# Optimization experiments

Hardware: AMD Instinct MI355X
Metric: run time of the kernel (lower is better)

The kernel has to match this reference:

```python
import jax, jax.numpy as jnp
import numpy as np
import math

B, TQ, TK, C, H, DFF = 4, 1024, 1024, 1024, 16, 4096
DK = C // H
EPS = 1e-12


def _mha(x_q, x_kv, wq, bq, wk, bk, wv, bv, wo, bo, mask):
    Bq, Tq, Cq = x_q.shape
    Tk = x_kv.shape[1]
    q = (x_q @ wq + bq).reshape(Bq, Tq, H, DK).transpose(0, 2, 1, 3)  # [B,H,Tq,dk]
    k = (x_kv @ wk + bk).reshape(Bq, Tk, H, DK).transpose(0, 2, 1, 3)
    v = (x_kv @ wv + bv).reshape(Bq, Tk, H, DK).transpose(0, 2, 1, 3)
    scores = jnp.einsum('bhqd,bhkd->bhqk', q, k) * (1.0 / math.sqrt(DK))
    if mask is not None:
        scores = jnp.where(mask, scores, jnp.asarray(-1e9, scores.dtype))
    attn = jax.nn.softmax(scores, axis=-1)
    o = jnp.einsum('bhqk,bhkd->bhqd', attn, v).transpose(0, 2, 1, 3).reshape(Bq, Tq, Cq)
    return o @ wo + bo


def _ln(x, g, b):
    mu = jnp.mean(x, axis=-1, keepdims=True)
    var = jnp.mean(jnp.square(x - mu), axis=-1, keepdims=True)
    return (x - mu) * jax.lax.rsqrt(var + EPS) * g + b


def setup_inputs() -> dict:
    key = jax.random.key(0)
    ks = iter(jax.random.split(key, 32))
    s = 0.02
    inp = {}
    inp['src'] = jax.random.normal(next(ks), (B, TK, C), jnp.float32)
    inp['dst'] = jax.random.normal(next(ks), (B, TQ, C), jnp.float32)
    inp['src_mask'] = jnp.ones((B, 1, 1, TK), dtype=bool)  # key-padding mask (all valid)
    inp['dst_mask'] = jnp.tril(jnp.ones((TQ, TQ), dtype=bool))[None, None]  # causal
    for p in ['sa', 'ca']:
        for n in ['wq', 'wk', 'wv', 'wo']:
            inp[f'{p}_{n}'] = jax.random.normal(next(ks), (C, C), jnp.float32) * s
        for n in ['bq', 'bk', 'bv', 'bo']:
            inp[f'{p}_{n}'] = jnp.zeros((C,), jnp.float32)
    inp['ffn_w1'] = jax.random.normal(next(ks), (C, DFF), jnp.float32) * s
    inp['ffn_b1'] = jnp.zeros((DFF,), jnp.float32)
    inp['ffn_w2'] = jax.random.normal(next(ks), (DFF, C), jnp.float32) * s
    inp['ffn_b2'] = jnp.zeros((C,), jnp.float32)
    for i in ['1', '2', '3']:
        inp[f'ln{i}_g'] = jnp.ones((C,), jnp.float32)
        inp[f'ln{i}_b'] = jnp.zeros((C,), jnp.float32)
    return inp


def reference(src, dst, src_mask, dst_mask,
              sa_wq, sa_wk, sa_wv, sa_wo, sa_bq, sa_bk, sa_bv, sa_bo,
              ca_wq, ca_wk, ca_wv, ca_wo, ca_bq, ca_bk, ca_bv, ca_bo,
              ffn_w1, ffn_b1, ffn_w2, ffn_b2,
              ln1_g, ln1_b, ln2_g, ln2_b, ln3_g, ln3_b):
    # post-LN decoder layer, eval mode (dropout is identity)
    sa = _mha(dst, dst, sa_wq, sa_bq, sa_wk, sa_bk, sa_wv, sa_bv, sa_wo, sa_bo, dst_mask)
    y = _ln(dst + sa, ln1_g, ln1_b)
    ca = _mha(y, src, ca_wq, ca_bq, ca_wk, ca_bk, ca_wv, ca_bv, ca_wo, ca_bo, src_mask)
    y = _ln(y + ca, ln2_g, ln2_b)
    ff = jax.nn.gelu(y @ ffn_w1 + ffn_b1, approximate=False) @ ffn_w2 + ffn_b2
    return _ln(y + ff, ln3_g, ln3_b)
```

## Files before the change

kernel.cpp:

```cpp
#include <hip/hip_runtime.h>
#include <math.h>

typedef __attribute__((ext_vector_type(4))) float f32x4;
typedef __attribute__((ext_vector_type(8))) __bf16 bf16x8;
typedef __attribute__((ext_vector_type(8))) short short8;

#define DEV __device__ __forceinline__

DEV short f2bfs(float f) {
    unsigned u = __builtin_bit_cast(unsigned, f);
    unsigned r = (u + 0x7FFFu + ((u >> 16) & 1u)) >> 16;
    return (short)r;
}

DEV f32x4 mfma16(bf16x8 a, bf16x8 b, f32x4 c) {
    return __builtin_amdgcn_mfma_f32_16x16x32_bf16(a, b, c, 0, 0, 0);
}

DEV void gload_lds16(const void* g, void* l) {
    __builtin_amdgcn_global_load_lds((const __attribute__((address_space(1))) void*)g,
                                     (__attribute__((address_space(3))) void*)l, 16, 0, 0);
}

__global__ __launch_bounds__(256) void wtrans(const float* __restrict__ Win,
                                              short* __restrict__ Wout,
                                              int Kd, int Nd) {
    __shared__ float Tt[32][33];
    const int tx = threadIdx.x & 31, ty = threadIdx.x >> 5;
    const int k0 = blockIdx.y * 32, n0 = blockIdx.x * 32;
#pragma unroll
    for (int rr = 0; rr < 4; ++rr) {
        int k = ty * 4 + rr;
        Tt[k][tx] = Win[(size_t)(k0 + k) * Nd + n0 + tx];
    }
    __syncthreads();
#pragma unroll
    for (int rr = 0; rr < 4; ++rr) {
        int n = ty * 4 + rr;
        Wout[(size_t)(n0 + n) * Kd + k0 + tx] = f2bfs(Tt[tx][n]);
    }
}

struct WPtrs { const float* p[8]; };

__global__ __launch_bounds__(256) void wtrans8(WPtrs wp, short* __restrict__ out) {
    const float* __restrict__ Win = wp.p[blockIdx.z];
    short* __restrict__ Wout = out + (size_t)blockIdx.z * (1024 * 1024);
    __shared__ float Tt[32][33];
    const int tx = threadIdx.x & 31, ty = threadIdx.x >> 5;
    const int k0 = blockIdx.y * 32, n0 = blockIdx.x * 32;
#pragma unroll
    for (int rr = 0; rr < 4; ++rr) {
        int k = ty * 4 + rr;
        Tt[k][tx] = Win[(size_t)(k0 + k) * 1024 + n0 + tx];
    }
    __syncthreads();
#pragma unroll
    for (int rr = 0; rr < 4; ++rr) {
        int n = ty * 4 + rr;
        Wout[(size_t)(n0 + n) * 1024 + k0 + tx] = f2bfs(Tt[tx][n]);
    }
}

__global__ __launch_bounds__(256) void conv_bf16(const float* __restrict__ X,
                                                 short* __restrict__ Y, int n4) {
    int i = blockIdx.x * 256 + threadIdx.x;
    if (i < n4) {
        float4 v = ((const float4*)X)[i];
        short4 o;
        o.x = f2bfs(v.x); o.y = f2bfs(v.y); o.z = f2bfs(v.z); o.w = f2bfs(v.w);
        ((short4*)Y)[i] = o;
    }
}

template <int BM, int EPI>
__global__ __launch_bounds__(256) void gemm_bt(const short* __restrict__ A,
                                               const short* __restrict__ BT,
                                               const float* __restrict__ b0,
                                               const float* __restrict__ b1,
                                               const float* __restrict__ b2,
                                               void* __restrict__ o0,
                                               void* __restrict__ o1,
                                               void* __restrict__ o2,
                                               int M, int N, int K) {
    constexpr int IM = BM / 32;
    __shared__ __align__(16) short As[BM * 64];
    __shared__ __align__(16) short Bs[128 * 64];
    const int tid = threadIdx.x, lane = tid & 63, w = tid >> 6;
    const int m0 = blockIdx.y * BM, n0 = blockIdx.x * 128;
    const int wm = (w & 1) * (BM / 2), wn = (w >> 1) * 64;
    const int rl = lane & 15, rg = lane >> 4;
    f32x4 acc[IM][4] = {};
    const char* Ab = (const char*)A;
    const char* Bb = (const char*)BT;

    for (int k0 = 0; k0 < K; k0 += 64) {
        __syncthreads();
#pragma unroll
        for (int r = 0; r < BM / 32; ++r) {
            int lo = (w * (BM / 32) + r) * 1024 + lane * 16;
            int row = lo >> 7, cp = (lo >> 4) & 7, c = (cp - row) & 7;
            gload_lds16(Ab + ((size_t)(m0 + row) * K + k0 + c * 8) * 2, (char*)As + lo);
        }
#pragma unroll
        for (int r = 0; r < 4; ++r) {
            int lo = (w * 4 + r) * 1024 + lane * 16;
            int row = lo >> 7, cp = (lo >> 4) & 7, c = (cp - row) & 7;
            gload_lds16(Bb + ((size_t)(n0 + row) * K + k0 + c * 8) * 2, (char*)Bs + lo);
        }
        __syncthreads();
        bf16x8 af[IM][2], bfr[4][2];
#pragma unroll
        for (int i = 0; i < IM; i++) {
            int row = wm + i * 16 + rl;
#pragma unroll
            for (int kk = 0; kk < 2; kk++)
                af[i][kk] = *(const bf16x8*)(As + row * 64 + ((((kk << 2) | rg) + row) & 7) * 8);
        }
#pragma unroll
        for (int j = 0; j < 4; j++) {
            int row = wn + j * 16 + rl;
#pragma unroll
            for (int kk = 0; kk < 2; kk++)
                bfr[j][kk] = *(const bf16x8*)(Bs + row * 64 + ((((kk << 2) | rg) + row) & 7) * 8);
        }
#pragma unroll
        for (int i = 0; i < IM; i++)
#pragma unroll
            for (int j = 0; j < 4; j++) {
                acc[i][j] = mfma16(af[i][0], bfr[j][0], acc[i][j]);
                acc[i][j] = mfma16(af[i][1], bfr[j][1], acc[i][j]);
            }
    }

#pragma unroll
    for (int i = 0; i < IM; i++) {
        int gm0 = m0 + wm + i * 16 + rg * 4;
#pragma unroll
        for (int j = 0; j < 4; j++) {
            int gn = n0 + wn + j * 16 + rl;
            if (EPI == 0) {
                float bv = b0[gn];
#pragma unroll
                for (int r = 0; r < 4; r++)
                    ((float*)o0)[(size_t)(gm0 + r) * N + gn] = acc[i][j][r] + bv;
            } else if (EPI == 2) {
                float bv = b0[gn];
#pragma unroll
                for (int r = 0; r < 4; r++) {
                    float v = acc[i][j][r] + bv;
                    float g = 0.5f * v * (1.0f + erff(v * 0.70710678118654752f));
                    ((short*)o0)[(size_t)(gm0 + r) * N + gn] = f2bfs(g);
                }
            } else {
                int seg = gn >> 10, n1 = gn & 1023, h = n1 >> 6, d = n1 & 63;
                int b = gm0 >> 10, t0 = gm0 & 1023;
                bool isV = (EPI == 1) ? (seg == 2) : (seg == 1);
                const float* bp = (EPI == 1) ? (seg == 0 ? b0 : (seg == 1 ? b1 : b2))
                                             : (seg == 0 ? b0 : b1);
                float bv = bp[n1];
                if (!isV) {
                    short* hp = (short*)((EPI == 1) ? (seg == 0 ? o0 : o1) : o0);
                    size_t base = ((size_t)(b * 16 + h) * 1024 + t0) * 64 + d;
#pragma unroll
                    for (int r = 0; r < 4; r++)
                        hp[base + (size_t)r * 64] = f2bfs(acc[i][j][r] + bv);
                } else {
                    short* vp = (short*)((EPI == 1) ? o2 : o1);
                    short4 pk;
                    pk.x = f2bfs(acc[i][j][0] + bv);
                    pk.y = f2bfs(acc[i][j][1] + bv);
                    pk.z = f2bfs(acc[i][j][2] + bv);
                    pk.w = f2bfs(acc[i][j][3] + bv);
                    *(short4*)(vp + ((size_t)(b * 16 + h) * 64 + d) * 1024 + t0) = pk;
                }
            }
        }
    }
}

template <bool CAUSAL>
__global__ __launch_bounds__(256) void attn_fused(const short* __restrict__ Qh,
                                                  const short* __restrict__ Kh,
                                                  const short* __restrict__ VTh,
                                                  short* __restrict__ Out, int TKn) {
    __shared__ __align__(16) short Ks[32 * 72];
    __shared__ __align__(16) short Vts[64 * 40];
    __shared__ __align__(16) short Ps[4 * 16 * 40];
    const int tid = threadIdx.x, lane = tid & 63, w = tid >> 6;
    const int rl = lane & 15, rg = lane >> 4;
    const int bh = blockIdx.y, b = bh >> 4, h = bh & 15;
    const int q0 = blockIdx.x * 64;
    const size_t qbase = (size_t)bh * 1024 * 64;
    const size_t kbase = (size_t)bh * (size_t)TKn * 64;

    bf16x8 qf[2];
    {
        int qrow = q0 + w * 16 + rl;
        qf[0] = *(const bf16x8*)(Qh + qbase + (size_t)qrow * 64 + rg * 8);
        qf[1] = *(const bf16x8*)(Qh + qbase + (size_t)qrow * 64 + 32 + rg * 8);
    }
    f32x4 o[4] = {};
    float mrow[4] = {-1e30f, -1e30f, -1e30f, -1e30f};
    float lrow[4] = {0.f, 0.f, 0.f, 0.f};

    const int nkt = CAUSAL ? (q0 >> 5) + 2 : (TKn >> 5);
    for (int kt = 0; kt < nkt; ++kt) {
        __syncthreads();
        {
            int key = tid >> 3, dg = tid & 7;
            *(bf16x8*)(Ks + key * 72 + dg * 8) =
                *(const bf16x8*)(Kh + kbase + (size_t)(kt * 32 + key) * 64 + dg * 8);
            int d = tid >> 2, kg = tid & 3;
            *(bf16x8*)(Vts + d * 40 + kg * 8) =
                *(const bf16x8*)(VTh + kbase + (size_t)d * TKn + kt * 32 + kg * 8);
        }
        __syncthreads();
        f32x4 s[2];
#pragma unroll
        for (int ch = 0; ch < 2; ++ch) {
            f32x4 z = {};
            bf16x8 kb0 = *(const bf16x8*)(Ks + (ch * 16 + rl) * 72 + rg * 8);
            bf16x8 kb1 = *(const bf16x8*)(Ks + (ch * 16 + rl) * 72 + 32 + rg * 8);
            z = mfma16(qf[0], kb0, z);
            z = mfma16(qf[1], kb1, z);
            s[ch] = z;
        }
        float alpha[4];
        short* Pw = Ps + w * 640;
#pragma unroll
        for (int r = 0; r < 4; ++r) {
            float s0 = s[0][r] * 0.125f, s1 = s[1][r] * 0.125f;
            if (CAUSAL) {
                int qr = q0 + w * 16 + rg * 4 + r;
                if (kt * 32 + rl > qr) s0 = -1e30f;
                if (kt * 32 + 16 + rl > qr) s1 = -1e30f;
            }
            float mx = fmaxf(s0, s1);
            mx = fmaxf(mx, __shfl_xor(mx, 1));
            mx = fmaxf(mx, __shfl_xor(mx, 2));
            mx = fmaxf(mx, __shfl_xor(mx, 4));
            mx = fmaxf(mx, __shfl_xor(mx, 8));
            float mn = fmaxf(mrow[r], mx);
            float al = __expf(mrow[r] - mn);
            mrow[r] = mn;
            float p0 = __expf(s0 - mn), p1 = __expf(s1 - mn);
            float rs = p0 + p1;
            rs += __shfl_xor(rs, 1);
            rs += __shfl_xor(rs, 2);
            rs += __shfl_xor(rs, 4);
            rs += __shfl_xor(rs, 8);
            lrow[r] = lrow[r] * al + rs;
            alpha[r] = al;
            Pw[(rg * 4 + r) * 40 + rl] = f2bfs(p0);
            Pw[(rg * 4 + r) * 40 + 16 + rl] = f2bfs(p1);
        }
#pragma unroll
        for (int j = 0; j < 4; j++)
#pragma unroll
            for (int r = 0; r < 4; r++) o[j][r] *= alpha[r];
        bf16x8 pa = *(const bf16x8*)(Ps + w * 640 + rl * 40 + rg * 8);
#pragma unroll
        for (int j = 0; j < 4; j++) {
            bf16x8 vb = *(const bf16x8*)(Vts + (j * 16 + rl) * 40 + rg * 8);
            o[j] = mfma16(pa, vb, o[j]);
        }
    }
    float inv[4];
#pragma unroll
    for (int r = 0; r < 4; r++) inv[r] = 1.0f / lrow[r];
#pragma unroll
    for (int j = 0; j < 4; j++) {
#pragma unroll
        for (int r = 0; r < 4; r++) {
            int row = q0 + w * 16 + rg * 4 + r;
            int col = h * 64 + j * 16 + rl;
            Out[((size_t)b * 1024 + row) * 1024 + col] = f2bfs(o[j][r] * inv[r]);
        }
    }
}

__global__ __launch_bounds__(256) void ln_fused(const float* __restrict__ X,
                                                const float* __restrict__ R,
                                                const float* __restrict__ gam,
                                                const float* __restrict__ bet,
                                                float* __restrict__ Yf,
                                                short* __restrict__ Yb) {
    const int row = blockIdx.x, tid = threadIdx.x;
    const int lane = tid & 63, w = tid >> 6;
    const float* xr = X + (size_t)row * 1024;
    const float* rr = R + (size_t)row * 1024;
    float4 xv = ((const float4*)xr)[tid];
    float4 rv = ((const float4*)rr)[tid];
    float v0 = xv.x + rv.x, v1 = xv.y + rv.y, v2 = xv.z + rv.z, v3 = xv.w + rv.w;
    float s = v0 + v1 + v2 + v3;
    float ss = v0 * v0 + v1 * v1 + v2 * v2 + v3 * v3;
#pragma unroll
    for (int off = 1; off < 64; off <<= 1) {
        s += __shfl_xor(s, off);
        ss += __shfl_xor(ss, off);
    }
    __shared__ float sred[4], ssred[4];
    if (lane == 0) { sred[w] = s; ssred[w] = ss; }
    __syncthreads();
    s = sred[0] + sred[1] + sred[2] + sred[3];
    ss = ssred[0] + ssred[1] + ssred[2] + ssred[3];
    float mu = s * (1.0f / 1024.0f);
    float var = ss * (1.0f / 1024.0f) - mu * mu;
    float rsq = rsqrtf(var + 1e-12f);
    float4 gv = ((const float4*)gam)[tid];
    float4 bv = ((const float4*)bet)[tid];
    float y0 = (v0 - mu) * rsq * gv.x + bv.x;
    float y1 = (v1 - mu) * rsq * gv.y + bv.y;
    float y2 = (v2 - mu) * rsq * gv.z + bv.z;
    float y3 = (v3 - mu) * rsq * gv.w + bv.w;
    float4 yo = {y0, y1, y2, y3};
    ((float4*)(Yf + (size_t)row * 1024))[tid] = yo;
    if (Yb) {
        short4 ob;
        ob.x = f2bfs(y0); ob.y = f2bfs(y1); ob.z = f2bfs(y2); ob.w = f2bfs(y3);
        ((short4*)(Yb + (size_t)row * 1024))[tid] = ob;
    }
}

extern "C" void kernel_launch(void* const* d_in, const int* in_sizes, int n_in,
                              void* d_out, int out_size, void* d_ws, size_t ws_size,
                              hipStream_t stream) {
    const float* src = (const float*)d_in[0];
    const float* dst = (const float*)d_in[1];
    const float* sa_wq = (const float*)d_in[4];
    const float* sa_wk = (const float*)d_in[5];
    const float* sa_wv = (const float*)d_in[6];
    const float* sa_wo = (const float*)d_in[7];
    const float* sa_bq = (const float*)d_in[8];
    const float* sa_bk = (const float*)d_in[9];
    const float* sa_bv = (const float*)d_in[10];
    const float* sa_bo = (const float*)d_in[11];
    const float* ca_wq = (const float*)d_in[12];
    const float* ca_wk = (const float*)d_in[13];
    const float* ca_wv = (const float*)d_in[14];
    const float* ca_wo = (const float*)d_in[15];
    const float* ca_bq = (const float*)d_in[16];
    const float* ca_bk = (const float*)d_in[17];
    const float* ca_bv = (const float*)d_in[18];
    const float* ca_bo = (const float*)d_in[19];
    const float* ffn_w1 = (const float*)d_in[20];
    const float* ffn_b1 = (const float*)d_in[21];
    const float* ffn_w2 = (const float*)d_in[22];
    const float* ffn_b2 = (const float*)d_in[23];
    const float* ln1g = (const float*)d_in[24];
    const float* ln1b = (const float*)d_in[25];
    const float* ln2g = (const float*)d_in[26];
    const float* ln2b = (const float*)d_in[27];
    const float* ln3g = (const float*)d_in[28];
    const float* ln3b = (const float*)d_in[29];

    char* ws = (char*)d_ws;
    size_t off = 0;
    auto alloc = [&](size_t n) { size_t o = off; off = (off + n + 255) & ~(size_t)255; return o; };

    const size_t szW = (size_t)1024 * 1024 * 2;
    short* wT = (short*)(ws + alloc(8 * szW));
    short* w1T = (short*)(ws + alloc((size_t)4096 * 1024 * 2));
    short* w2T = (short*)(ws + alloc((size_t)1024 * 4096 * 2));
    const size_t szAct2 = (size_t)4096 * 1024 * 2;
    const size_t szAct4 = (size_t)4096 * 1024 * 4;
    short* dstb = (short*)(ws + alloc(szAct2));
    short* srcb = (short*)(ws + alloc(szAct2));
    short* Qh = (short*)(ws + alloc(szAct2));
    short* Kh = (short*)(ws + alloc(szAct2));
    short* VTh = (short*)(ws + alloc(szAct2));
    short* attnb = (short*)(ws + alloc(szAct2));
    float* tmp = (float*)(ws + alloc(szAct4));
    float* y1f = (float*)(ws + alloc(szAct4));
    short* y1b = (short*)(ws + alloc(szAct2));
    float* y2f = (float*)(ws + alloc(szAct4));
    short* y2b = (short*)(ws + alloc(szAct2));
    short* ffnh = (short*)(ws + alloc((size_t)4096 * 4096 * 2));

    short* sa_wqkvT = wT;
    short* sa_woT = wT + 3 * (size_t)1048576;
    short* ca_wqT = wT + 4 * (size_t)1048576;
    short* ca_wkvT = wT + 5 * (size_t)1048576;
    short* ca_woT = wT + 7 * (size_t)1048576;

    dim3 blk(256);

    WPtrs wp = {{sa_wq, sa_wk, sa_wv, sa_wo, ca_wq, ca_wk, ca_wv, ca_wo}};
    wtrans8<<<dim3(32, 32, 8), blk, 0, stream>>>(wp, wT);
    wtrans<<<dim3(128, 32), blk, 0, stream>>>(ffn_w1, w1T, 1024, 4096);
    wtrans<<<dim3(32, 128), blk, 0, stream>>>(ffn_w2, w2T, 4096, 1024);
    conv_bf16<<<4096, blk, 0, stream>>>(dst, dstb, 1048576);
    conv_bf16<<<4096, blk, 0, stream>>>(src, srcb, 1048576);

    gemm_bt<128, 1><<<dim3(24, 32), blk, 0, stream>>>(dstb, sa_wqkvT, sa_bq, sa_bk, sa_bv,
                                                      Qh, Kh, VTh, 4096, 3072, 1024);
    attn_fused<true><<<dim3(16, 64), blk, 0, stream>>>(Qh, Kh, VTh, attnb, 1024);
    gemm_bt<64, 0><<<dim3(8, 64), blk, 0, stream>>>(attnb, sa_woT, sa_bo, nullptr, nullptr,
                                                    tmp, nullptr, nullptr, 4096, 1024, 1024);
    ln_fused<<<4096, blk, 0, stream>>>(dst, tmp, ln1g, ln1b, y1f, y1b);

    gemm_bt<64, 1><<<dim3(8, 64), blk, 0, stream>>>(y1b, ca_wqT, ca_bq, nullptr, nullptr,
                                                    Qh, nullptr, nullptr, 4096, 1024, 1024);
    gemm_bt<128, 3><<<dim3(16, 32), blk, 0, stream>>>(srcb, ca_wkvT, ca_bk, ca_bv, nullptr,
                                                      Kh, VTh, nullptr, 4096, 2048, 1024);
    attn_fused<false><<<dim3(16, 64), blk, 0, stream>>>(Qh, Kh, VTh, attnb, 1024);
    gemm_bt<64, 0><<<dim3(8, 64), blk, 0, stream>>>(attnb, ca_woT, ca_bo, nullptr, nullptr,
                                                    tmp, nullptr, nullptr, 4096, 1024, 1024);
    ln_fused<<<4096, blk, 0, stream>>>(y1f, tmp, ln2g, ln2b, y2f, y2b);

    gemm_bt<128, 2><<<dim3(32, 32), blk, 0, stream>>>(y2b, w1T, ffn_b1, nullptr, nullptr,
                                                      ffnh, nullptr, nullptr, 4096, 4096, 1024);
    gemm_bt<64, 0><<<dim3(8, 64), blk, 0, stream>>>(ffnh, w2T, ffn_b2, nullptr, nullptr,
                                                    tmp, nullptr, nullptr, 4096, 1024, 4096);
    ln_fused<<<4096, blk, 0, stream>>>(y2f, tmp, ln3g, ln3b, (float*)d_out, nullptr);

    (void)in_sizes; (void)n_in; (void)out_size; (void)ws_size;
}
```

Before: 624.2 us.

## Rewrite attention to read K/V fragments from global with 64-key tiles

The attention kernel no longer stages K and V^T tiles in shared memory behind two block barriers per step. Instead each wave loads its MFMA operand fragments straight from global memory and processes 64 keys per iteration instead of 32. The causal mask is now applied only on the last key tile. The 1/sqrt(dk) scale is folded into the Q projection epilogue, and probabilities are converted to bf16 by truncation instead of rounding. This removes barrier and LDS traffic, at the cost of four waves reading the same K/V data redundantly through cache, higher register pressure, and slightly less accurate P rounding.

```diff
diff --git a/kernel.cpp b/kernel.cpp
--- a/kernel.cpp
+++ b/kernel.cpp
@@ -11,6 +11,10 @@
     unsigned u = __builtin_bit_cast(unsigned, f);
     unsigned r = (u + 0x7FFFu + ((u >> 16) & 1u)) >> 16;
     return (short)r;
+}
+
+DEV short f2bft(float f) {
+    return (short)(__builtin_bit_cast(unsigned, f) >> 16);
 }
 
 DEV f32x4 mfma16(bf16x8 a, bf16x8 b, f32x4 c) {
@@ -159,12 +163,13 @@
                 const float* bp = (EPI == 1) ? (seg == 0 ? b0 : (seg == 1 ? b1 : b2))
                                              : (seg == 0 ? b0 : b1);
                 float bv = bp[n1];
+                float qs = (EPI == 1 && seg == 0) ? 0.125f : 1.0f;
                 if (!isV) {
                     short* hp = (short*)((EPI == 1) ? (seg == 0 ? o0 : o1) : o0);
                     size_t base = ((size_t)(b * 16 + h) * 1024 + t0) * 64 + d;
 #pragma unroll
                     for (int r = 0; r < 4; r++)
-                        hp[base + (size_t)r * 64] = f2bfs(acc[i][j][r] + bv);
+                        hp[base + (size_t)r * 64] = f2bfs((acc[i][j][r] + bv) * qs);
                 } else {
                     short* vp = (short*)((EPI == 1) ? o2 : o1);
                     short4 pk;
@@ -180,63 +185,72 @@
 }
 
 template <bool CAUSAL>
-__global__ __launch_bounds__(256) void attn_fused(const short* __restrict__ Qh,
-                                                  const short* __restrict__ Kh,
-                                                  const short* __restrict__ VTh,
-                                                  short* __restrict__ Out, int TKn) {
-    __shared__ __align__(16) short Ks[32 * 72];
-    __shared__ __align__(16) short Vts[64 * 40];
-    __shared__ __align__(16) short Ps[4 * 16 * 40];
+__global__ __launch_bounds__(256, 4) void attn2(const short* __restrict__ Qh,
+                                                const short* __restrict__ Kh,
+                                                const short* __restrict__ VTh,
+                                                short* __restrict__ Out, int TKn) {
+    __shared__ __align__(16) short Ps[4][16 * 66 + 8];
     const int tid = threadIdx.x, lane = tid & 63, w = tid >> 6;
     const int rl = lane & 15, rg = lane >> 4;
     const int bh = blockIdx.y, b = bh >> 4, h = bh & 15;
     const int q0 = blockIdx.x * 64;
-    const size_t qbase = (size_t)bh * 1024 * 64;
-    const size_t kbase = (size_t)bh * (size_t)TKn * 64;
-
-    bf16x8 qf[2];
-    {
-        int qrow = q0 + w * 16 + rl;
-        qf[0] = *(const bf16x8*)(Qh + qbase + (size_t)qrow * 64 + rg * 8);
-        qf[1] = *(const bf16x8*)(Qh + qbase + (size_t)qrow * 64 + 32 + rg * 8);
-    }
+    const short* Qp = Qh + (size_t)bh * 1024 * 64;
+    const short* Kp = Kh + (size_t)bh * (size_t)TKn * 64;
+    const short* Vp = VTh + (size_t)bh * (size_t)TKn * 64;
+
+    const int qrow = q0 + w * 16 + rl;
+    const bf16x8 qf0 = *(const bf16x8*)(Qp + (size_t)qrow * 64 + rg * 8);
+    const bf16x8 qf1 = *(const bf16x8*)(Qp + (size_t)qrow * 64 + 32 + rg * 8);
+
     f32x4 o[4] = {};
     float mrow[4] = {-1e30f, -1e30f, -1e30f, -1e30f};
     float lrow[4] = {0.f, 0.f, 0.f, 0.f};
 
-    const int nkt = CAUSAL ? (q0 >> 5) + 2 : (TKn >> 5);
+    int kofs[4], vofs[4];
+#pragma unroll
+    for (int ch = 0; ch < 4; ++ch) kofs[ch] = (ch * 16 + rl) * 64 + rg * 8;
+#pragma unroll
+    for (int j = 0; j < 4; ++j) vofs[j] = (j * 16 + rl) * TKn + rg * 8;
+
+    short* Pw = &Ps[w][0];
+    const int nkt = CAUSAL ? blockIdx.x + 1 : (TKn >> 6);
+
     for (int kt = 0; kt < nkt; ++kt) {
-        __syncthreads();
-        {
-            int key = tid >> 3, dg = tid & 7;
-            *(bf16x8*)(Ks + key * 72 + dg * 8) =
-                *(const bf16x8*)(Kh + kbase + (size_t)(kt * 32 + key) * 64 + dg * 8);
-            int d = tid >> 2, kg = tid & 3;
-            *(bf16x8*)(Vts + d * 40 + kg * 8) =
-                *(const bf16x8*)(VTh + kbase + (size_t)d * TKn + kt * 32 + kg * 8);
-        }
-        __syncthreads();
-        f32x4 s[2];
-#pragma unroll
-        for (int ch = 0; ch < 2; ++ch) {
+        const short* kB = Kp + kt * 4096;
+        bf16x8 kf[4][2];
+#pragma unroll
+        for (int ch = 0; ch < 4; ++ch) {
+            kf[ch][0] = *(const bf16x8*)(kB + kofs[ch]);
+            kf[ch][1] = *(const bf16x8*)(kB + kofs[ch] + 32);
+        }
+        f32x4 s[4];
+#pragma unroll
+        for (int ch = 0; ch < 4; ++ch) {
             f32x4 z = {};
-            bf16x8 kb0 = *(const bf16x8*)(Ks + (ch * 16 + rl) * 72 + rg * 8);
-            bf16x8 kb1 = *(const bf16x8*)(Ks + (ch * 16 + rl) * 72 + 32 + rg * 8);
-            z = mfma16(qf[0], kb0, z);
-            z = mfma16(qf[1], kb1, z);
+            z = mfma16(qf0, kf[ch][0], z);
+            z = mfma16(qf1, kf[ch][1], z);
             s[ch] = z;
         }
+        bf16x8 vf[4][2];
+#pragma unroll
+        for (int j = 0; j < 4; ++j) {
+            vf[j][0] = *(const bf16x8*)(Vp + vofs[j] + kt * 64);
+            vf[j][1] = *(const bf16x8*)(Vp + vofs[j] + kt * 64 + 32);
+        }
+        const bool domask = CAUSAL && (kt == nkt - 1);
         float alpha[4];
-        short* Pw = Ps + w * 640;
 #pragma unroll
         for (int r = 0; r < 4; ++r) {
-            float s0 = s[0][r] * 0.125f, s1 = s[1][r] * 0.125f;
-            if (CAUSAL) {
+            float s0 = s[0][r], s1 = s[1][r], s2 = s[2][r], s3 = s[3][r];
+            if (domask) {
                 int qr = q0 + w * 16 + rg * 4 + r;
-                if (kt * 32 + rl > qr) s0 = -1e30f;
-                if (kt * 32 + 16 + rl > qr) s1 = -1e30f;
+                int kb = kt * 64 + rl;
+                if (kb > qr) s0 = -1e30f;
+                if (kb + 16 > qr) s1 = -1e30f;
+                if (kb + 32 > qr) s2 = -1e30f;
+                if (kb + 48 > qr) s3 = -1e30f;
             }
-            float mx = fmaxf(s0, s1);
+            float mx = fmaxf(fmaxf(s0, s1), fmaxf(s2, s3));
             mx = fmaxf(mx, __shfl_xor(mx, 1));
             mx = fmaxf(mx, __shfl_xor(mx, 2));
             mx = fmaxf(mx, __shfl_xor(mx, 4));
@@ -245,25 +259,30 @@
             float al = __expf(mrow[r] - mn);
             mrow[r] = mn;
             float p0 = __expf(s0 - mn), p1 = __expf(s1 - mn);
-            float rs = p0 + p1;
+            float p2 = __expf(s2 - mn), p3 = __expf(s3 - mn);
+            float rs = (p0 + p1) + (p2 + p3);
             rs += __shfl_xor(rs, 1);
             rs += __shfl_xor(rs, 2);
             rs += __shfl_xor(rs, 4);
             rs += __shfl_xor(rs, 8);
             lrow[r] = lrow[r] * al + rs;
             alpha[r] = al;
-            Pw[(rg * 4 + r) * 40 + rl] = f2bfs(p0);
-            Pw[(rg * 4 + r) * 40 + 16 + rl] = f2bfs(p1);
+            int prow = (rg * 4 + r) * 66;
+            Pw[prow + rl] = f2bft(p0);
+            Pw[prow + 16 + rl] = f2bft(p1);
+            Pw[prow + 32 + rl] = f2bft(p2);
+            Pw[prow + 48 + rl] = f2bft(p3);
         }
 #pragma unroll
         for (int j = 0; j < 4; j++)
 #pragma unroll
             for (int r = 0; r < 4; r++) o[j][r] *= alpha[r];
-        bf16x8 pa = *(const bf16x8*)(Ps + w * 640 + rl * 40 + rg * 8);
+        bf16x8 pa0 = *(const bf16x8*)(Pw + rl * 66 + rg * 8);
+        bf16x8 pa1 = *(const bf16x8*)(Pw + rl * 66 + 32 + rg * 8);
 #pragma unroll
         for (int j = 0; j < 4; j++) {
-            bf16x8 vb = *(const bf16x8*)(Vts + (j * 16 + rl) * 40 + rg * 8);
-            o[j] = mfma16(pa, vb, o[j]);
+            o[j] = mfma16(pa0, vf[j][0], o[j]);
+            o[j] = mfma16(pa1, vf[j][1], o[j]);
         }
     }
     float inv[4];
@@ -395,7 +414,7 @@
 
     gemm_bt<128, 1><<<dim3(24, 32), blk, 0, stream>>>(dstb, sa_wqkvT, sa_bq, sa_bk, sa_bv,
                                                       Qh, Kh, VTh, 4096, 3072, 1024);
-    attn_fused<true><<<dim3(16, 64), blk, 0, stream>>>(Qh, Kh, VTh, attnb, 1024);
+    attn2<true><<<dim3(16, 64), blk, 0, stream>>>(Qh, Kh, VTh, attnb, 1024);
     gemm_bt<64, 0><<<dim3(8, 64), blk, 0, stream>>>(attnb, sa_woT, sa_bo, nullptr, nullptr,
                                                     tmp, nullptr, nullptr, 4096, 1024, 1024);
     ln_fused<<<4096, blk, 0, stream>>>(dst, tmp, ln1g, ln1b, y1f, y1b);
@@ -404,7 +423,7 @@
                                                     Qh, nullptr, nullptr, 4096, 1024, 1024);
     gemm_bt<128, 3><<<dim3(16, 32), blk, 0, stream>>>(srcb, ca_wkvT, ca_bk, ca_bv, nullptr,
                                                       Kh, VTh, nullptr, 4096, 2048, 1024);
-    attn_fused<false><<<dim3(16, 64), blk, 0, stream>>>(Qh, Kh, VTh, attnb, 1024);
+    attn2<false><<<dim3(16, 64), blk, 0, stream>>>(Qh, Kh, VTh, attnb, 1024);
     gemm_bt<64, 0><<<dim3(8, 64), blk, 0, stream>>>(attnb, ca_woT, ca_bo, nullptr, nullptr,
                                                     tmp, nullptr, nullptr, 4096, 1024, 1024);
     ln_fused<<<4096, blk, 0, stream>>>(y1f, tmp, ln2g, ln2b, y2f, y2b);
```

After: 696.1 us. 11.5% more time.
